# Kernel tuning notes

Hardware: AMD Instinct MI355X
Metric: run time of the kernel (lower is better)

The kernel has to match this reference:

```python
import jax, jax.numpy as jnp
import numpy as np

WSCALE = 0.05  # keep ReLU MLP activations in a sane range


def setup_inputs() -> dict:
    key = jax.random.key(0)
    ks = jax.random.split(key, 9)
    B, D, H = 2048, 64, 512
    return {
        "x": jax.random.normal(ks[0], (B, D), dtype=jnp.float32),
        "W1": jax.random.normal(ks[1], (H, D), dtype=jnp.float32) * WSCALE,
        "b1": jax.random.normal(ks[2], (H,), dtype=jnp.float32) * WSCALE,
        "W2": jax.random.normal(ks[3], (H, H), dtype=jnp.float32) * WSCALE,
        "b2": jax.random.normal(ks[4], (H,), dtype=jnp.float32) * WSCALE,
        "W3": jax.random.normal(ks[5], (H, H), dtype=jnp.float32) * WSCALE,
        "b3": jax.random.normal(ks[6], (H,), dtype=jnp.float32) * WSCALE,
        "W4": jax.random.normal(ks[7], (D, H), dtype=jnp.float32) * WSCALE,
        "b4": jax.random.normal(ks[8], (D,), dtype=jnp.float32) * WSCALE,
    }


def reference(x, W1, b1, W2, b2, W3, b3, W4, b4):
    # Score network: ReLU MLP (weights stored PyTorch-style [out, in]).
    a1 = x @ W1.T + b1          # [B, H]
    h1 = jax.nn.relu(a1)
    a2 = h1 @ W2.T + b2
    h2 = jax.nn.relu(a2)
    a3 = h2 @ W3.T + b3
    h3 = jax.nn.relu(a3)
    s = h3 @ W4.T + b4          # [B, D] score

    # Divergence = trace of Jacobian ds/dx per sample.
    # Per-sample J = W4 @ diag(m3) @ W3 @ diag(m2) @ W2 @ diag(m1) @ W1,
    # with m_k = 1[a_k > 0] (ReLU derivative; 0 at 0 like torch autograd).
    m1 = (a1 > 0).astype(x.dtype)
    m2 = (a2 > 0).astype(x.dtype)
    m3 = (a3 > 0).astype(x.dtype)
    T = m1[:, :, None] * W1[None, :, :]                 # [B, H, D]
    T = m2[:, :, None] * jnp.einsum('ij,bjd->bid', W2, T)  # [B, H, D]
    T = m3[:, :, None] * jnp.einsum('ij,bjd->bid', W3, T)  # [B, H, D]
    div = jnp.einsum('dj,bjd->b', W4, T)                # trace of J, [B]

    # Hyvarinen score: 0.5 * ||s||^2 + div
    val = 0.5 * jnp.sum(s * s, axis=1) + div
    return val
```

## Files before the change

### kernel.cpp

```cpp
#include <hip/hip_runtime.h>
#include <stdint.h>


typedef __attribute__((ext_vector_type(8))) short short8;
typedef __attribute__((ext_vector_type(4))) float f32x4;

union U16x8 {
  uint4 u;
  short8 s;
};

__device__ __forceinline__ uint16_t f2bf(float f) {
  uint32_t u = __float_as_uint(f);
  uint32_t lsb = (u >> 16) & 1u;
  u += 0x7FFFu + lsb;
  return (uint16_t)(u >> 16);
}

__device__ __forceinline__ void lds_load16(const uint4* gsrc, uint4* ldst) {
  __builtin_amdgcn_global_load_lds(
      (const __attribute__((address_space(1))) void*)gsrc,
      (__attribute__((address_space(3))) void*)ldst, 16, 0, 0);
}

__global__ __launch_bounds__(256) void convert_kernel(
    const float* __restrict__ W1, const float* __restrict__ W2,
    const float* __restrict__ W3, const float* __restrict__ W4,
    uint16_t* __restrict__ A2swz, uint16_t* __restrict__ A3swz,
    uint16_t* __restrict__ B1swz, uint16_t* __restrict__ B4swz,
    float* __restrict__ W2Tf, float* __restrict__ W3Tf,
    float* __restrict__ W1Tf, float* __restrict__ W4Tf) {
  const int i = blockIdx.x * 256 + threadIdx.x;
  if (i < 262144) {
    const int e = i;
    const int f = e >> 3, j = e & 7;
    const int lane = f & 63, fk = f >> 6;
    const int kc = fk & 15, r16 = fk >> 4;
    const int l15 = lane & 15, quad = lane >> 4;
    const int row = r16 * 16 + l15, col = kc * 32 + quad * 8 + j;
    A2swz[e] = f2bf(W2[row * 512 + col]);
  } else if (i < 524288) {
    const int e = i - 262144;
    const int f = e >> 3, j = e & 7;
    const int lane = f & 63, fk = f >> 6;
    const int kc = fk & 15, r16 = fk >> 4;
    const int l15 = lane & 15, quad = lane >> 4;
    const int row = r16 * 16 + l15, col = kc * 32 + quad * 8 + j;
    A3swz[e] = f2bf(W3[col * 512 + row]);
  } else if (i < 557056) {
    const int e = i - 524288;
    const int f = e >> 3, j = e & 7;
    const int lane = f & 63, fk = f >> 6;
    const int kc = fk >> 2, jt = fk & 3;
    const int l15 = lane & 15, quad = lane >> 4;
    const int d = jt * 16 + l15, col = kc * 32 + quad * 8 + j;
    B1swz[e] = f2bf(W1[col * 64 + d]);
  } else if (i < 589824) {
    const int e = i - 557056;
    const int f = e >> 3, j = e & 7;
    const int lane = f & 63, fk = f >> 6;
    const int kc = fk >> 2, jt = fk & 3;
    const int l15 = lane & 15, quad = lane >> 4;
    const int d = jt * 16 + l15, col = kc * 32 + quad * 8 + j;
    B4swz[e] = f2bf(W4[d * 512 + col]);
  } else if (i < 851968) {
    const int e = i - 589824;
    const int k = e >> 9, jj = e & 511;
    W2Tf[e] = W2[jj * 512 + k];
  } else if (i < 1114112) {
    const int e = i - 851968;
    const int k = e >> 9, jj = e & 511;
    W3Tf[e] = W3[jj * 512 + k];
  } else if (i < 1146880) {
    const int e = i - 1114112;
    const int k = e >> 9, jj = e & 511;
    W1Tf[e] = W1[jj * 64 + k];
  } else if (i < 1179648) {
    const int e = i - 1146880;
    const int k = e >> 6, d = e & 63;
    W4Tf[e] = W4[d * 512 + k];
  }
}

__device__ __forceinline__ void relu_store_mask(
    float acc[8], float4 (*hdst)[2], uint32_t* __restrict__ mbase,
    int t, int lane, int wv) {
#pragma unroll
  for (int s = 0; s < 8; ++s) {
    const unsigned long long bal = __ballot(acc[s] > 0.f);
    if (lane == 0) {
      uint2 w2;
      w2.x = (uint32_t)bal;
      w2.y = (uint32_t)(bal >> 32);
      *(uint2*)(mbase + (size_t)s * 16 + 2 * wv) = w2;
    }
  }
  float4 r0, r1;
  r0.x = acc[0] > 0.f ? acc[0] : 0.f;
  r0.y = acc[1] > 0.f ? acc[1] : 0.f;
  r0.z = acc[2] > 0.f ? acc[2] : 0.f;
  r0.w = acc[3] > 0.f ? acc[3] : 0.f;
  r1.x = acc[4] > 0.f ? acc[4] : 0.f;
  r1.y = acc[5] > 0.f ? acc[5] : 0.f;
  r1.z = acc[6] > 0.f ? acc[6] : 0.f;
  r1.w = acc[7] > 0.f ? acc[7] : 0.f;
  hdst[t][0] = r0;
  hdst[t][1] = r1;
}

__global__ __launch_bounds__(512) void forward_kernel(
    const float* __restrict__ x,
    const float* __restrict__ W1Tf, const float* __restrict__ b1,
    const float* __restrict__ W2Tf, const float* __restrict__ b2,
    const float* __restrict__ W3Tf, const float* __restrict__ b3,
    const float* __restrict__ W4Tf, const float* __restrict__ b4,
    uint32_t* __restrict__ m1p, uint32_t* __restrict__ m2p,
    uint32_t* __restrict__ m3p, float* __restrict__ out) {
  __shared__ float4 xs[64][2];
  __shared__ float4 hA[512][2];
  __shared__ float4 hB[512][2];
  const int t = threadIdx.x;
  const int lane = t & 63, wv = t >> 6;
  const int b0 = blockIdx.x * 8;

  {
    const int k = t >> 3, s = t & 7;
    ((float*)&xs[k][0])[s] = x[(size_t)(b0 + s) * 64 + k];
  }
  __syncthreads();

  float acc[8];

  {
    const float bj = b1[t];
#pragma unroll
    for (int s = 0; s < 8; ++s) acc[s] = bj;
#pragma unroll 8
    for (int k = 0; k < 64; ++k) {
      const float w = W1Tf[(size_t)k * 512 + t];
      const float4 h0 = xs[k][0], h1 = xs[k][1];
      acc[0] = fmaf(w, h0.x, acc[0]); acc[1] = fmaf(w, h0.y, acc[1]);
      acc[2] = fmaf(w, h0.z, acc[2]); acc[3] = fmaf(w, h0.w, acc[3]);
      acc[4] = fmaf(w, h1.x, acc[4]); acc[5] = fmaf(w, h1.y, acc[5]);
      acc[6] = fmaf(w, h1.z, acc[6]); acc[7] = fmaf(w, h1.w, acc[7]);
    }
    relu_store_mask(acc, hA, m1p + (size_t)b0 * 16, t, lane, wv);
  }
  __syncthreads();

  {
    const float bj = b2[t];
#pragma unroll
    for (int s = 0; s < 8; ++s) acc[s] = bj;
#pragma unroll 8
    for (int k = 0; k < 512; ++k) {
      const float w = W2Tf[(size_t)k * 512 + t];
      const float4 h0 = hA[k][0], h1 = hA[k][1];
      acc[0] = fmaf(w, h0.x, acc[0]); acc[1] = fmaf(w, h0.y, acc[1]);
      acc[2] = fmaf(w, h0.z, acc[2]); acc[3] = fmaf(w, h0.w, acc[3]);
      acc[4] = fmaf(w, h1.x, acc[4]); acc[5] = fmaf(w, h1.y, acc[5]);
      acc[6] = fmaf(w, h1.z, acc[6]); acc[7] = fmaf(w, h1.w, acc[7]);
    }
    relu_store_mask(acc, hB, m2p + (size_t)b0 * 16, t, lane, wv);
  }
  __syncthreads();

  {
    const float bj = b3[t];
#pragma unroll
    for (int s = 0; s < 8; ++s) acc[s] = bj;
#pragma unroll 8
    for (int k = 0; k < 512; ++k) {
      const float w = W3Tf[(size_t)k * 512 + t];
      const float4 h0 = hB[k][0], h1 = hB[k][1];
      acc[0] = fmaf(w, h0.x, acc[0]); acc[1] = fmaf(w, h0.y, acc[1]);
      acc[2] = fmaf(w, h0.z, acc[2]); acc[3] = fmaf(w, h0.w, acc[3]);
      acc[4] = fmaf(w, h1.x, acc[4]); acc[5] = fmaf(w, h1.y, acc[5]);
      acc[6] = fmaf(w, h1.z, acc[6]); acc[7] = fmaf(w, h1.w, acc[7]);
    }
    relu_store_mask(acc, hA, m3p + (size_t)b0 * 16, t, lane, wv);
  }
  __syncthreads();

  {
    const int s = wv, d = lane;
    const float* hf = (const float*)&hA[0][0];
    float a4 = b4[d];
#pragma unroll 8
    for (int k = 0; k < 512; ++k)
      a4 = fmaf(W4Tf[(size_t)k * 64 + d], hf[k * 8 + s], a4);
    float sq = a4 * a4;
#pragma unroll
    for (int off = 32; off; off >>= 1) sq += __shfl_down(sq, off, 64);
    if (lane == 0) out[b0 + s] = 0.5f * sq;
  }
}

__device__ __forceinline__ void expand_mask(uint32_t byte8, uint32_t mk[4]) {
#pragma unroll
  for (int i = 0; i < 4; ++i) {
    mk[i] = (((byte8 >> (2 * i)) & 1u) ? 0x0000FFFFu : 0u) |
            (((byte8 >> (2 * i + 1)) & 1u) ? 0xFFFF0000u : 0u);
  }
}

__global__ __launch_bounds__(256, 2) void div_kernel(
    const uint4* __restrict__ A2swz, const uint4* __restrict__ A3swz,
    const uint4* __restrict__ B1swz, const uint4* __restrict__ B4swz,
    const uint32_t* __restrict__ m1p, const uint32_t* __restrict__ m2p,
    const uint32_t* __restrict__ m3p, float* __restrict__ out) {
  __shared__ uint4 sfrag[2][16][64];
  const int t = threadIdx.x;
  const int lane = t & 63, wv = t >> 6;
  const int l15 = lane & 15, quad = lane >> 4;
  (void)l15;
  const int g4 = blockIdx.x;
  const int rowB0 = blockIdx.y * 64;
  const int b = g4 * 4 + wv;
  const int r16b = blockIdx.y * 4;

  const uint4* sb = (wv == 0) ? A2swz : (wv == 1) ? A3swz : (wv == 2) ? B1swz : B4swz;

  f32x4 accC[4][4], accG[4][4];
#pragma unroll
  for (int it = 0; it < 4; ++it)
#pragma unroll
    for (int jt = 0; jt < 4; ++jt) {
      accC[it][jt] = (f32x4){0.f, 0.f, 0.f, 0.f};
      accG[it][jt] = (f32x4){0.f, 0.f, 0.f, 0.f};
    }

  const uint32_t* m1w = m1p + (size_t)b * 16;
  const uint32_t* m3w = m3p + (size_t)b * 16;

  auto stage = [&](int sbuf, int kc) {
#pragma unroll
    for (int q = 0; q < 4; ++q) {
      const size_t off = (wv < 2)
          ? ((size_t)((r16b + q) * 16 + kc) * 64 + lane)
          : ((size_t)(kc * 4 + q) * 64 + lane);
      lds_load16(sb + off, &sfrag[sbuf][wv * 4 + q][0]);
    }
  };

  stage(0, 0);
  uint32_t m1d_n = __builtin_amdgcn_readfirstlane(m1w[0]);
  uint32_t m3d_n = __builtin_amdgcn_readfirstlane(m3w[0]);
  __syncthreads();

  int buf = 0;
#pragma unroll 1
  for (int kc = 0; kc < 16; ++kc) {
    if (kc < 15) stage(buf ^ 1, kc + 1);

    const uint32_t m1d = m1d_n;
    const uint32_t m3d = m3d_n;
    if (kc < 15) {
      m1d_n = __builtin_amdgcn_readfirstlane(m1w[kc + 1]);
      m3d_n = __builtin_amdgcn_readfirstlane(m3w[kc + 1]);
    }

    uint4 a2[4], a3[4], u1[4], u4[4];
#pragma unroll
    for (int q = 0; q < 4; ++q) {
      a2[q] = sfrag[buf][q][lane];
      a3[q] = sfrag[buf][4 + q][lane];
      u1[q] = sfrag[buf][8 + q][lane];
      u4[q] = sfrag[buf][12 + q][lane];
    }

    uint32_t mk1[4], mk3[4];
    expand_mask((m1d >> (quad * 8)) & 0xFFu, mk1);
    expand_mask((m3d >> (quad * 8)) & 0xFFu, mk3);

    short8 bC[4];
#pragma unroll
    for (int jt = 0; jt < 4; ++jt) {
      U16x8 u;
      u.u = u1[jt];
      u.u.x &= mk1[0]; u.u.y &= mk1[1]; u.u.z &= mk1[2]; u.u.w &= mk1[3];
      bC[jt] = u.s;
    }
#pragma unroll
    for (int it = 0; it < 4; ++it) {
      U16x8 ua;
      ua.u = a2[it];
      const short8 af = ua.s;
#pragma unroll
      for (int jt = 0; jt < 4; ++jt)
        accC[it][jt] = __builtin_amdgcn_mfma_f32_16x16x32_bf16(af, bC[jt], accC[it][jt], 0, 0, 0);
    }
    short8 bG[4];
#pragma unroll
    for (int jt = 0; jt < 4; ++jt) {
      U16x8 u;
      u.u = u4[jt];
      u.u.x &= mk3[0]; u.u.y &= mk3[1]; u.u.z &= mk3[2]; u.u.w &= mk3[3];
      bG[jt] = u.s;
    }
#pragma unroll
    for (int it = 0; it < 4; ++it) {
      U16x8 ua;
      ua.u = a3[it];
      const short8 af = ua.s;
#pragma unroll
      for (int jt = 0; jt < 4; ++jt)
        accG[it][jt] = __builtin_amdgcn_mfma_f32_16x16x32_bf16(af, bG[jt], accG[it][jt], 0, 0, 0);
    }
    __syncthreads();
    buf ^= 1;
  }

  const uint32_t* m2w = m2p + (size_t)b * 16;
  float dsum = 0.f;
#pragma unroll
  for (int it = 0; it < 4; ++it) {
    const int rloc = it * 16 + quad * 4;
    const uint32_t md = m2w[(rowB0 + rloc) >> 5];
    const uint32_t bits = (md >> (rloc & 31)) & 0xFu;
    const float w0 = (bits & 1u) ? 1.f : 0.f;
    const float w1 = (bits & 2u) ? 1.f : 0.f;
    const float w2 = (bits & 4u) ? 1.f : 0.f;
    const float w3 = (bits & 8u) ? 1.f : 0.f;
#pragma unroll
    for (int jt = 0; jt < 4; ++jt) {
      dsum = fmaf(w0, accC[it][jt][0] * accG[it][jt][0], dsum);
      dsum = fmaf(w1, accC[it][jt][1] * accG[it][jt][1], dsum);
      dsum = fmaf(w2, accC[it][jt][2] * accG[it][jt][2], dsum);
      dsum = fmaf(w3, accC[it][jt][3] * accG[it][jt][3], dsum);
    }
  }
#pragma unroll
  for (int off = 32; off; off >>= 1) dsum += __shfl_down(dsum, off, 64);
  if (lane == 0) atomicAdd(out + b, dsum);
}

extern "C" void kernel_launch(void* const* d_in, const int* in_sizes, int n_in,
                              void* d_out, int out_size, void* d_ws, size_t ws_size,
                              hipStream_t stream) {
  const float* x  = (const float*)d_in[0];
  const float* W1 = (const float*)d_in[1];
  const float* b1 = (const float*)d_in[2];
  const float* W2 = (const float*)d_in[3];
  const float* b2 = (const float*)d_in[4];
  const float* W3 = (const float*)d_in[5];
  const float* b3 = (const float*)d_in[6];
  const float* W4 = (const float*)d_in[7];
  const float* b4 = (const float*)d_in[8];
  float* out = (float*)d_out;

  char* ws = (char*)d_ws;
  uint16_t* A2swz = (uint16_t*)(ws + 0);
  uint16_t* A3swz = (uint16_t*)(ws + 524288);
  uint16_t* B1swz = (uint16_t*)(ws + 1048576);
  uint16_t* B4swz = (uint16_t*)(ws + 1114112);
  float*    W2Tf  = (float*)(ws + 1179648);
  float*    W3Tf  = (float*)(ws + 2228224);
  float*    W1Tf  = (float*)(ws + 3276800);
  float*    W4Tf  = (float*)(ws + 3407872);
  uint32_t* m1p   = (uint32_t*)(ws + 3538944);
  uint32_t* m2p   = (uint32_t*)(ws + 3670016);
  uint32_t* m3p   = (uint32_t*)(ws + 3801088);
  if (ws_size < 3932160) return;

  convert_kernel<<<4608, 256, 0, stream>>>(W1, W2, W3, W4,
                                           A2swz, A3swz, B1swz, B4swz,
                                           W2Tf, W3Tf, W1Tf, W4Tf);
  forward_kernel<<<256, 512, 0, stream>>>(x, W1Tf, b1, W2Tf, b2, W3Tf, b3,
                                          W4Tf, b4, m1p, m2p, m3p, out);
  div_kernel<<<dim3(512, 8), 256, 0, stream>>>((const uint4*)A2swz,
                                               (const uint4*)A3swz,
                                               (const uint4*)B1swz,
                                               (const uint4*)B4swz,
                                               m1p, m2p, m3p, out);
}
```

Baseline: 303.5 us.

## Triple-buffer div kernel staging, cache masks in LDS, halve forward rows per block

The divergence kernel moves from double to triple buffering of LDS fragments. It waits with explicit vmcnt counts and raw s_barrier instead of full __syncthreads, so global-to-LDS loads run two stages ahead. Per-sample masks are loaded into LDS once at the start, replacing per-iteration global reads. The forward kernel now handles 4 samples per block over 512 blocks instead of 8 over 256, to improve parallelism across CUs, at the cost of reading the weight matrices twice as many times.

```diff
diff --git a/kernel.cpp b/kernel.cpp
--- a/kernel.cpp
+++ b/kernel.cpp
@@ -82,11 +82,11 @@
   }
 }
 
-__device__ __forceinline__ void relu_store_mask(
-    float acc[8], float4 (*hdst)[2], uint32_t* __restrict__ mbase,
+__device__ __forceinline__ void relu_store_mask4(
+    float acc[4], float (*hdst)[4], uint32_t* __restrict__ mbase,
     int t, int lane, int wv) {
 #pragma unroll
-  for (int s = 0; s < 8; ++s) {
+  for (int s = 0; s < 4; ++s) {
     const unsigned long long bal = __ballot(acc[s] > 0.f);
     if (lane == 0) {
       uint2 w2;
@@ -95,17 +95,12 @@
       *(uint2*)(mbase + (size_t)s * 16 + 2 * wv) = w2;
     }
   }
-  float4 r0, r1;
-  r0.x = acc[0] > 0.f ? acc[0] : 0.f;
-  r0.y = acc[1] > 0.f ? acc[1] : 0.f;
-  r0.z = acc[2] > 0.f ? acc[2] : 0.f;
-  r0.w = acc[3] > 0.f ? acc[3] : 0.f;
-  r1.x = acc[4] > 0.f ? acc[4] : 0.f;
-  r1.y = acc[5] > 0.f ? acc[5] : 0.f;
-  r1.z = acc[6] > 0.f ? acc[6] : 0.f;
-  r1.w = acc[7] > 0.f ? acc[7] : 0.f;
-  hdst[t][0] = r0;
-  hdst[t][1] = r1;
+  float4 r;
+  r.x = acc[0] > 0.f ? acc[0] : 0.f;
+  r.y = acc[1] > 0.f ? acc[1] : 0.f;
+  r.z = acc[2] > 0.f ? acc[2] : 0.f;
+  r.w = acc[3] > 0.f ? acc[3] : 0.f;
+  *(float4*)&hdst[t][0] = r;
 }
 
 __global__ __launch_bounds__(512) void forward_kernel(
@@ -116,79 +111,72 @@
     const float* __restrict__ W4Tf, const float* __restrict__ b4,
     uint32_t* __restrict__ m1p, uint32_t* __restrict__ m2p,
     uint32_t* __restrict__ m3p, float* __restrict__ out) {
-  __shared__ float4 xs[64][2];
-  __shared__ float4 hA[512][2];
-  __shared__ float4 hB[512][2];
+  __shared__ float xs[64][4];
+  __shared__ float hA[512][4];
+  __shared__ float hB[512][4];
   const int t = threadIdx.x;
   const int lane = t & 63, wv = t >> 6;
-  const int b0 = blockIdx.x * 8;
-
-  {
-    const int k = t >> 3, s = t & 7;
-    ((float*)&xs[k][0])[s] = x[(size_t)(b0 + s) * 64 + k];
+  const int b0 = blockIdx.x * 4;
+
+  if (t < 256) {
+    const int k = t >> 2, s = t & 3;
+    xs[k][s] = x[(size_t)(b0 + s) * 64 + k];
   }
   __syncthreads();
 
-  float acc[8];
+  float acc[4];
 
   {
     const float bj = b1[t];
 #pragma unroll
-    for (int s = 0; s < 8; ++s) acc[s] = bj;
+    for (int s = 0; s < 4; ++s) acc[s] = bj;
 #pragma unroll 8
     for (int k = 0; k < 64; ++k) {
       const float w = W1Tf[(size_t)k * 512 + t];
-      const float4 h0 = xs[k][0], h1 = xs[k][1];
-      acc[0] = fmaf(w, h0.x, acc[0]); acc[1] = fmaf(w, h0.y, acc[1]);
-      acc[2] = fmaf(w, h0.z, acc[2]); acc[3] = fmaf(w, h0.w, acc[3]);
-      acc[4] = fmaf(w, h1.x, acc[4]); acc[5] = fmaf(w, h1.y, acc[5]);
-      acc[6] = fmaf(w, h1.z, acc[6]); acc[7] = fmaf(w, h1.w, acc[7]);
-    }
-    relu_store_mask(acc, hA, m1p + (size_t)b0 * 16, t, lane, wv);
+      const float4 h = *(const float4*)&xs[k][0];
+      acc[0] = fmaf(w, h.x, acc[0]); acc[1] = fmaf(w, h.y, acc[1]);
+      acc[2] = fmaf(w, h.z, acc[2]); acc[3] = fmaf(w, h.w, acc[3]);
+    }
+    relu_store_mask4(acc, hA, m1p + (size_t)b0 * 16, t, lane, wv);
   }
   __syncthreads();
 
   {
     const float bj = b2[t];
 #pragma unroll
-    for (int s = 0; s < 8; ++s) acc[s] = bj;
+    for (int s = 0; s < 4; ++s) acc[s] = bj;
 #pragma unroll 8
     for (int k = 0; k < 512; ++k) {
       const float w = W2Tf[(size_t)k * 512 + t];
-      const float4 h0 = hA[k][0], h1 = hA[k][1];
-      acc[0] = fmaf(w, h0.x, acc[0]); acc[1] = fmaf(w, h0.y, acc[1]);
-      acc[2] = fmaf(w, h0.z, acc[2]); acc[3] = fmaf(w, h0.w, acc[3]);
-      acc[4] = fmaf(w, h1.x, acc[4]); acc[5] = fmaf(w, h1.y, acc[5]);
-      acc[6] = fmaf(w, h1.z, acc[6]); acc[7] = fmaf(w, h1.w, acc[7]);
-    }
-    relu_store_mask(acc, hB, m2p + (size_t)b0 * 16, t, lane, wv);
+      const float4 h = *(const float4*)&hA[k][0];
+      acc[0] = fmaf(w, h.x, acc[0]); acc[1] = fmaf(w, h.y, acc[1]);
+      acc[2] = fmaf(w, h.z, acc[2]); acc[3] = fmaf(w, h.w, acc[3]);
+    }
+    relu_store_mask4(acc, hB, m2p + (size_t)b0 * 16, t, lane, wv);
   }
   __syncthreads();
 
   {
     const float bj = b3[t];
 #pragma unroll
-    for (int s = 0; s < 8; ++s) acc[s] = bj;
+    for (int s = 0; s < 4; ++s) acc[s] = bj;
 #pragma unroll 8
     for (int k = 0; k < 512; ++k) {
       const float w = W3Tf[(size_t)k * 512 + t];
-      const float4 h0 = hB[k][0], h1 = hB[k][1];
-      acc[0] = fmaf(w, h0.x, acc[0]); acc[1] = fmaf(w, h0.y, acc[1]);
-      acc[2] = fmaf(w, h0.z, acc[2]); acc[3] = fmaf(w, h0.w, acc[3]);
-      acc[4] = fmaf(w, h1.x, acc[4]); acc[5] = fmaf(w, h1.y, acc[5]);
-      acc[6] = fmaf(w, h1.z, acc[6]); acc[7] = fmaf(w, h1.w, acc[7]);
-    }
-    relu_store_mask(acc, hA, m3p + (size_t)b0 * 16, t, lane, wv);
+      const float4 h = *(const float4*)&hB[k][0];
+      acc[0] = fmaf(w, h.x, acc[0]); acc[1] = fmaf(w, h.y, acc[1]);
+      acc[2] = fmaf(w, h.z, acc[2]); acc[3] = fmaf(w, h.w, acc[3]);
+    }
+    relu_store_mask4(acc, hA, m3p + (size_t)b0 * 16, t, lane, wv);
   }
   __syncthreads();
 
-  {
+  if (wv < 4) {
     const int s = wv, d = lane;
-    const float* hf = (const float*)&hA[0][0];
     float a4 = b4[d];
 #pragma unroll 8
     for (int k = 0; k < 512; ++k)
-      a4 = fmaf(W4Tf[(size_t)k * 64 + d], hf[k * 8 + s], a4);
+      a4 = fmaf(W4Tf[(size_t)k * 64 + d], hA[k][s], a4);
     float sq = a4 * a4;
 #pragma unroll
     for (int off = 32; off; off >>= 1) sq += __shfl_down(sq, off, 64);
@@ -209,11 +197,11 @@
     const uint4* __restrict__ B1swz, const uint4* __restrict__ B4swz,
     const uint32_t* __restrict__ m1p, const uint32_t* __restrict__ m2p,
     const uint32_t* __restrict__ m3p, float* __restrict__ out) {
-  __shared__ uint4 sfrag[2][16][64];
+  __shared__ uint4 sfrag[3][16][64];
+  __shared__ uint32_t smask[4][2][16];
   const int t = threadIdx.x;
   const int lane = t & 63, wv = t >> 6;
-  const int l15 = lane & 15, quad = lane >> 4;
-  (void)l15;
+  const int quad = lane >> 4;
   const int g4 = blockIdx.x;
   const int rowB0 = blockIdx.y * 64;
   const int b = g4 * 4 + wv;
@@ -230,8 +218,12 @@
       accG[it][jt] = (f32x4){0.f, 0.f, 0.f, 0.f};
     }
 
-  const uint32_t* m1w = m1p + (size_t)b * 16;
-  const uint32_t* m3w = m3p + (size_t)b * 16;
+  {
+    const uint32_t* m1w = m1p + (size_t)b * 16;
+    const uint32_t* m3w = m3p + (size_t)b * 16;
+    if (lane < 16) smask[wv][0][lane] = m1w[lane];
+    else if (lane < 32) smask[wv][1][lane & 15] = m3w[lane & 15];
+  }
 
   auto stage = [&](int sbuf, int kc) {
 #pragma unroll
@@ -244,29 +236,27 @@
   };
 
   stage(0, 0);
-  uint32_t m1d_n = __builtin_amdgcn_readfirstlane(m1w[0]);
-  uint32_t m3d_n = __builtin_amdgcn_readfirstlane(m3w[0]);
-  __syncthreads();
-
-  int buf = 0;
+  stage(1, 1);
+  __builtin_amdgcn_sched_barrier(0);
+  asm volatile("s_waitcnt vmcnt(4)" ::: "memory");
+  __builtin_amdgcn_s_barrier();
+  __builtin_amdgcn_sched_barrier(0);
+
 #pragma unroll 1
   for (int kc = 0; kc < 16; ++kc) {
-    if (kc < 15) stage(buf ^ 1, kc + 1);
-
-    const uint32_t m1d = m1d_n;
-    const uint32_t m3d = m3d_n;
-    if (kc < 15) {
-      m1d_n = __builtin_amdgcn_readfirstlane(m1w[kc + 1]);
-      m3d_n = __builtin_amdgcn_readfirstlane(m3w[kc + 1]);
-    }
+    const int rb = kc % 3;
+    if (kc < 14) stage((kc + 2) % 3, kc + 2);
+
+    const uint32_t m1d = __builtin_amdgcn_readfirstlane(smask[wv][0][kc]);
+    const uint32_t m3d = __builtin_amdgcn_readfirstlane(smask[wv][1][kc]);
 
     uint4 a2[4], a3[4], u1[4], u4[4];
 #pragma unroll
     for (int q = 0; q < 4; ++q) {
-      a2[q] = sfrag[buf][q][lane];
-      a3[q] = sfrag[buf][4 + q][lane];
-      u1[q] = sfrag[buf][8 + q][lane];
-      u4[q] = sfrag[buf][12 + q][lane];
+      a2[q] = sfrag[rb][q][lane];
+      a3[q] = sfrag[rb][4 + q][lane];
+      u1[q] = sfrag[rb][8 + q][lane];
+      u4[q] = sfrag[rb][12 + q][lane];
     }
 
     uint32_t mk1[4], mk3[4];
@@ -307,8 +297,16 @@
       for (int jt = 0; jt < 4; ++jt)
         accG[it][jt] = __builtin_amdgcn_mfma_f32_16x16x32_bf16(af, bG[jt], accG[it][jt], 0, 0, 0);
     }
-    __syncthreads();
-    buf ^= 1;
+
+    if (kc < 14) {
+      asm volatile("s_waitcnt vmcnt(4)" ::: "memory");
+    } else if (kc == 14) {
+      asm volatile("s_waitcnt vmcnt(0)" ::: "memory");
+    }
+    if (kc < 15) {
+      __builtin_amdgcn_s_barrier();
+      __builtin_amdgcn_sched_barrier(0);
+    }
   }
 
   const uint32_t* m2w = m2p + (size_t)b * 16;
@@ -366,7 +364,7 @@
   convert_kernel<<<4608, 256, 0, stream>>>(W1, W2, W3, W4,
                                            A2swz, A3swz, B1swz, B4swz,
                                            W2Tf, W3Tf, W1Tf, W4Tf);
-  forward_kernel<<<256, 512, 0, stream>>>(x, W1Tf, b1, W2Tf, b2, W3Tf, b3,
+  forward_kernel<<<512, 512, 0, stream>>>(x, W1Tf, b1, W2Tf, b2, W3Tf, b3,
                                           W4Tf, b4, m1p, m2p, m3p, out);
   div_kernel<<<dim3(512, 8), 256, 0, stream>>>((const uint4*)A2swz,
                                                (const uint4*)A3swz,
```

After: 281.3 us. 7.3% less time.
